# Performance work log

Hardware: AMD Instinct MI355X
Metric: run time of the kernel (lower is better)

Reference implementation:

```python
import jax, jax.numpy as jnp
import numpy as np

N, E = 50000, 800000
IN_C, HID, OUT_C = 100, 128, 40
LAYERS, GROUPS, CODES = 3, 3, 16
BETA = 0.98
EPS = 1e-5


def setup_inputs() -> dict:
    key = jax.random.key(0)
    ks = jax.random.split(key, 16)
    lin = lambda k, i, o: (jax.random.normal(k, (i, o), jnp.float32) / np.sqrt(i)).astype(jnp.float32)
    d = {}
    d["x"] = jax.random.normal(ks[0], (N, IN_C), jnp.float32)
    d["src"] = jax.random.randint(ks[1], (E,), 0, N, jnp.int32)
    d["dst"] = jax.random.randint(ks[2], (E,), 0, N, jnp.int32)
    # SAGEConv params: lin_l (aggregated, with bias) and lin_r (root, no bias)
    d["W0a"], d["W0r"], d["b0"] = lin(ks[3], IN_C, HID), lin(ks[4], IN_C, HID), jnp.zeros((HID,), jnp.float32)
    d["W1a"], d["W1r"], d["b1"] = lin(ks[5], HID, HID), lin(ks[6], HID, HID), jnp.zeros((HID,), jnp.float32)
    d["W2a"], d["W2r"], d["b2"] = lin(ks[7], HID, HID), lin(ks[8], HID, HID), jnp.zeros((HID,), jnp.float32)
    # BatchNorm (eval mode: running stats) for first num_layers-1 = 2 layers
    d["bn_gamma"] = jnp.ones((2, HID), jnp.float32)
    d["bn_beta"] = jnp.zeros((2, HID), jnp.float32)
    d["bn_mean"] = jnp.zeros((2, HID), jnp.float32)
    d["bn_var"] = jnp.ones((2, HID), jnp.float32)
    # Residual VQ codebooks: [layer, group, num_codes, feature]
    d["codebooks"] = 0.1 * jax.random.normal(ks[9], (LAYERS, GROUPS, CODES, HID), jnp.float32)
    d["lin_W"] = lin(ks[10], HID, OUT_C)
    d["lin_b"] = jnp.zeros((OUT_C,), jnp.float32)
    return d


def _sage_conv(h, src, dst, Wa, Wr, b):
    # mean neighbor aggregation (PyG SAGEConv, aggr='mean')
    msg = h[src]                                              # [E, d]
    agg = jax.ops.segment_sum(msg, dst, num_segments=N)       # [N, d]
    deg = jax.ops.segment_sum(jnp.ones((E,), h.dtype), dst, num_segments=N)
    agg = agg / jnp.maximum(deg, 1.0)[:, None]
    return agg @ Wa + b + h @ Wr


def _rvq(h, cb):
    # residual vector quantization over GROUPS codebooks; cb: [G, K, D]
    res, quant, ids = h, jnp.zeros_like(h), []
    for g in range(GROUPS):
        c = cb[g]                                             # [K, D]
        d2 = (jnp.sum(res * res, -1, keepdims=True)
              - 2.0 * res @ c.T + jnp.sum(c * c, -1))          # [N, K]
        idx = jnp.argmin(d2, axis=-1)
        q = c[idx]
        quant = quant + q
        res = res - q
        ids.append(idx)
    sg = jax.lax.stop_gradient
    loss = (BETA * jnp.mean((h - sg(quant)) ** 2)
            + (1.0 - BETA) * jnp.mean((sg(h) - quant) ** 2))
    return loss, jnp.stack(ids, axis=1)                        # [N, G] int


def reference(x, src, dst, W0a, W0r, b0, W1a, W1r, b1, W2a, W2r, b2,
              bn_gamma, bn_beta, bn_mean, bn_var, codebooks, lin_W, lin_b):
    Ws = [(W0a, W0r, b0), (W1a, W1r, b1), (W2a, W2r, b2)]
    h = x
    total_loss = jnp.float32(0.0)
    id_list = []
    for i in range(LAYERS - 1):
        h = _sage_conv(h, src, dst, *Ws[i])
        h = (h - bn_mean[i]) * jax.lax.rsqrt(bn_var[i] + EPS) * bn_gamma[i] + bn_beta[i]
        h = jax.nn.relu(h)                                     # dropout: eval mode (identity)
        loss, ids = _rvq(h, codebooks[i])
        total_loss = total_loss + loss
        id_list.append(ids)
    h = _sage_conv(h, src, dst, *Ws[-1])
    loss, ids = _rvq(h, codebooks[-1])
    total_loss = total_loss + loss
    id_list.append(ids)
    out = h @ lin_W + lin_b
    return out, total_loss, jnp.concatenate(id_list, axis=1)
```

## Files before the change

### kernel.cpp

```cpp
#include <hip/hip_runtime.h>

#define NN 50000
#define HID 128
#define IN_C 100
#define OUT_C 40

__global__ __launch_bounds__(256)
void hist_kernel(const int* __restrict__ dst, int* __restrict__ deg, int E) {
    int e = blockIdx.x * 256 + threadIdx.x;
    if (e < E) atomicAdd(&deg[dst[e]], 1);
}

__global__ __launch_bounds__(256)
void chunk_sum_kernel(const int* __restrict__ deg, int* __restrict__ chunk_sums, int N) {
    __shared__ int s[256];
    const int t = threadIdx.x;
    const int i = blockIdx.x * 256 + t;
    s[t] = (i < N) ? deg[i] : 0;
    __syncthreads();
    for (int o = 128; o; o >>= 1) { if (t < o) s[t] += s[t + o]; __syncthreads(); }
    if (t == 0) chunk_sums[blockIdx.x] = s[0];
}

__global__ __launch_bounds__(256)
void chunk_scan_kernel(int* __restrict__ chunk_sums, int M) {
    __shared__ int s[256];
    const int t = threadIdx.x;
    int v = (t < M) ? chunk_sums[t] : 0;
    s[t] = v;
    __syncthreads();
    for (int o = 1; o < 256; o <<= 1) {
        int x = (t >= o) ? s[t - o] : 0;
        __syncthreads();
        s[t] += x;
        __syncthreads();
    }
    if (t < M) chunk_sums[t] = s[t] - v;
}

__global__ __launch_bounds__(256)
void chunk_apply_kernel(const int* __restrict__ deg, const int* __restrict__ chunk_sums,
                        int* __restrict__ row_start, int* __restrict__ cursor, int N) {
    __shared__ int s[256];
    const int t = threadIdx.x;
    const int i = blockIdx.x * 256 + t;
    int v = (i < N) ? deg[i] : 0;
    s[t] = v;
    __syncthreads();
    for (int o = 1; o < 256; o <<= 1) {
        int x = (t >= o) ? s[t - o] : 0;
        __syncthreads();
        s[t] += x;
        __syncthreads();
    }
    if (i < N) {
        int ex = chunk_sums[blockIdx.x] + s[t] - v;
        row_start[i] = ex;
        cursor[i] = ex;
        if (i == N - 1) row_start[N] = ex + v;
    }
}

__global__ __launch_bounds__(256)
void scatter_kernel(const int* __restrict__ src, const int* __restrict__ dst,
                    int* __restrict__ cursor, int* __restrict__ csr_src, int E) {
    int e = blockIdx.x * 256 + threadIdx.x;
    if (e < E) {
        int pos = atomicAdd(&cursor[dst[e]], 1);
        csr_src[pos] = src[e];
    }
}

__global__ __launch_bounds__(128)
void prep_pack(const float* __restrict__ Wa, const float* __restrict__ Wr,
               float2* __restrict__ wp) {
    const int k = blockIdx.x, col = threadIdx.x;
    float2 v;
    v.x = Wa[(size_t)k * HID + col];
    v.y = Wr[(size_t)k * HID + col];
    wp[(size_t)k * HID + col] = v;
}

template<int K, bool HAS_BN>
__global__ __launch_bounds__(512, 6)
void layer_fused(const float* __restrict__ h_in,
                 const int* __restrict__ row_start, const int* __restrict__ csr_src,
                 const float2* __restrict__ wp, const float* __restrict__ b,
                 const float* __restrict__ gamma, const float* __restrict__ beta,
                 const float* __restrict__ mean, const float* __restrict__ var,
                 const float* __restrict__ cb,
                 float* __restrict__ h_out,
                 float* __restrict__ ids_out, int id_col0,
                 double* __restrict__ loss_part) {
    __shared__ double s_agg[8][HID];
    __shared__ double s_h[8][HID];
    __shared__ float s_cb[3 * 16 * HID];
    const int t = threadIdx.x;
    const int w = t >> 6, lane = t & 63;
    const int n0 = blockIdx.x * 8;

    for (int idx = t; idx < 3 * 16 * HID; idx += 512) s_cb[idx] = cb[idx];

    {
        const int n = n0 + w;
        const int r0 = row_start[n], r1 = row_start[n + 1];
        const int f0 = 2 * lane;
        if (f0 < K) {
            double s0 = 0, s1 = 0, s2 = 0, s3 = 0, s4 = 0, s5 = 0, s6 = 0, s7 = 0;
            int i = r0;
            for (; i + 3 < r1; i += 4) {
                float2 v0 = *(const float2*)(h_in + (size_t)csr_src[i] * K + f0);
                float2 v1 = *(const float2*)(h_in + (size_t)csr_src[i + 1] * K + f0);
                float2 v2 = *(const float2*)(h_in + (size_t)csr_src[i + 2] * K + f0);
                float2 v3 = *(const float2*)(h_in + (size_t)csr_src[i + 3] * K + f0);
                s0 += (double)v0.x; s1 += (double)v0.y;
                s2 += (double)v1.x; s3 += (double)v1.y;
                s4 += (double)v2.x; s5 += (double)v2.y;
                s6 += (double)v3.x; s7 += (double)v3.y;
            }
            for (; i < r1; ++i) {
                float2 v = *(const float2*)(h_in + (size_t)csr_src[i] * K + f0);
                s0 += (double)v.x; s1 += (double)v.y;
            }
            const int deg = r1 - r0;
            const double dd = (double)(deg > 1 ? deg : 1);
            float2 root = *(const float2*)(h_in + (size_t)n * K + f0);
            s_agg[w][f0]     = ((s0 + s2) + (s4 + s6)) / dd;
            s_agg[w][f0 + 1] = ((s1 + s3) + (s5 + s7)) / dd;
            s_h[w][f0]     = (double)root.x;
            s_h[w][f0 + 1] = (double)root.y;
        }
    }
    __syncthreads();

    const int col = t & 127;
    const int p4 = t >> 7;
    double accA = (double)b[col];
    double accB = accA;
#pragma unroll 4
    for (int k = 0; k < K; ++k) {
        const float2 wv = wp[(size_t)k * HID + col];
        const double wa = (double)wv.x, wr = (double)wv.y;
        accA += s_agg[p4][k] * wa + s_h[p4][k] * wr;
        accB += s_agg[p4 + 4][k] * wa + s_h[p4 + 4][k] * wr;
    }
    __syncthreads();

    {
        double vA = accA, vB = accB;
        if (HAS_BN) {
            const double scale = (double)gamma[col] / sqrt((double)var[col] + 1e-5);
            const double shift = (double)beta[col] - (double)mean[col] * scale;
            vA = vA * scale + shift; vA = vA > 0.0 ? vA : 0.0;
            vB = vB * scale + shift; vB = vB > 0.0 ? vB : 0.0;
        }
        const float fA = (float)vA, fB = (float)vB;
        h_out[(size_t)(n0 + p4) * HID + col] = fA;
        h_out[(size_t)(n0 + p4 + 4) * HID + col] = fB;
        s_agg[p4][col] = (double)fA;
        s_agg[p4 + 4][col] = (double)fB;
    }
    __syncthreads();

    {
        double* res = &s_agg[w][0];
        double* s_ws = &s_h[0][0];
        const int n = n0 + w;
        const int k = lane & 15, q = lane >> 4;
        const int jbase = q * 32;
        const int rot = (k + 8 * q) & 31;

        for (int g = 0; g < 3; ++g) {
            const float* c = &s_cb[(g * 16 + k) * HID];
            double r0 = res[lane], r1 = res[lane + 64];
            double pr = r0 * r0 + r1 * r1;
            pr += __shfl_xor(pr, 1, 64);
            pr += __shfl_xor(pr, 2, 64);
            pr += __shfl_xor(pr, 4, 64);
            pr += __shfl_xor(pr, 8, 64);
            pr += __shfl_xor(pr, 16, 64);
            pr += __shfl_xor(pr, 32, 64);
            const float rr32 = (float)pr;

            double cc = 0.0, dot = 0.0;
#pragma unroll
            for (int j2 = 0; j2 < 32; ++j2) {
                const int j = jbase + ((j2 + rot) & 31);
                const double cj = (double)c[j];
                cc += cj * cj;
                dot += res[j] * cj;
            }
            cc += __shfl_xor(cc, 16, 64);
            cc += __shfl_xor(cc, 32, 64);
            dot += __shfl_xor(dot, 16, 64);
            dot += __shfl_xor(dot, 32, 64);

            const float cc32 = (float)cc;
            const float rc32 = (float)dot;
            const float t1 = rr32 - 2.0f * rc32;
            const float d2 = t1 + cc32;

            float bv = d2; int bk = k;
            {
                float ov; int ok;
                ov = __shfl_xor(bv, 1, 64); ok = __shfl_xor(bk, 1, 64);
                if (ov < bv || (ov == bv && ok < bk)) { bv = ov; bk = ok; }
                ov = __shfl_xor(bv, 2, 64); ok = __shfl_xor(bk, 2, 64);
                if (ov < bv || (ov == bv && ok < bk)) { bv = ov; bk = ok; }
                ov = __shfl_xor(bv, 4, 64); ok = __shfl_xor(bk, 4, 64);
                if (ov < bv || (ov == bv && ok < bk)) { bv = ov; bk = ok; }
                ov = __shfl_xor(bv, 8, 64); ok = __shfl_xor(bk, 8, 64);
                if (ov < bv || (ov == bv && ok < bk)) { bv = ov; bk = ok; }
            }
            if (lane == 0)
                ids_out[(size_t)n * 9 + id_col0 + g] = (float)bk;

            const float* cbest = &s_cb[(g * 16 + bk) * HID];
            res[lane]      -= (double)cbest[lane];
            res[lane + 64] -= (double)cbest[lane + 64];
        }
        double r0 = res[lane], r1 = res[lane + 64];
        double wl = r0 * r0 + r1 * r1;
        wl += __shfl_xor(wl, 1, 64);
        wl += __shfl_xor(wl, 2, 64);
        wl += __shfl_xor(wl, 4, 64);
        wl += __shfl_xor(wl, 8, 64);
        wl += __shfl_xor(wl, 16, 64);
        wl += __shfl_xor(wl, 32, 64);
        if (lane == 0) s_ws[w] = wl;
    }
    __syncthreads();
    if (t == 0) {
        const double* s_ws = &s_h[0][0];
        double s = 0.0;
#pragma unroll
        for (int i = 0; i < 8; i++) s += s_ws[i];
        loss_part[blockIdx.x] = s;
    }
}

__global__ __launch_bounds__(128)
void linear_kernel(const float* __restrict__ h, const float* __restrict__ W,
                   const float* __restrict__ b, float* __restrict__ out, int N) {
    constexpr int NODES = 32;
    __shared__ float s_w[HID * OUT_C];
    __shared__ float s_b[OUT_C];
    __shared__ float s_h[HID];
    const int t = threadIdx.x;
    for (int idx = t; idx < HID * OUT_C; idx += 128) s_w[idx] = W[idx];
    if (t < OUT_C) s_b[t] = b[t];
    __syncthreads();
    const int n0 = blockIdx.x * NODES;
    for (int ni = 0; ni < NODES; ++ni) {
        int n = n0 + ni;
        if (n >= N) break;
        s_h[t] = h[(size_t)n * HID + t];
        __syncthreads();
        if (t < OUT_C) {
            double acc = (double)s_b[t];
            for (int kk = 0; kk < HID; kk++)
                acc += (double)s_h[kk] * (double)s_w[kk * OUT_C + t];
            out[(size_t)n * OUT_C + t] = (float)acc;
        }
        __syncthreads();
    }
}

__global__ __launch_bounds__(256)
void finalize_kernel(const double* __restrict__ loss_part, int M,
                     float* __restrict__ out_loss) {
    __shared__ double s[256];
    const int t = threadIdx.x;
    double v = 0.0;
    for (int i = t; i < M; i += 256) v += loss_part[i];
    s[t] = v;
    __syncthreads();
    for (int off = 128; off; off >>= 1) {
        if (t < off) s[t] += s[t + off];
        __syncthreads();
    }
    if (t == 0) out_loss[0] = (float)(s[0] / ((double)NN * (double)HID));
}

extern "C" void kernel_launch(void* const* d_in, const int* in_sizes, int n_in,
                              void* d_out, int out_size, void* d_ws, size_t ws_size,
                              hipStream_t stream) {
    const float* x    = (const float*)d_in[0];
    const int*   src  = (const int*)d_in[1];
    const int*   dst  = (const int*)d_in[2];
    const float* W0a = (const float*)d_in[3];
    const float* W0r = (const float*)d_in[4];
    const float* b0  = (const float*)d_in[5];
    const float* W1a = (const float*)d_in[6];
    const float* W1r = (const float*)d_in[7];
    const float* b1  = (const float*)d_in[8];
    const float* W2a = (const float*)d_in[9];
    const float* W2r = (const float*)d_in[10];
    const float* b2  = (const float*)d_in[11];
    const float* bn_gamma = (const float*)d_in[12];
    const float* bn_beta  = (const float*)d_in[13];
    const float* bn_mean  = (const float*)d_in[14];
    const float* bn_var   = (const float*)d_in[15];
    const float* cb    = (const float*)d_in[16];
    const float* lin_W = (const float*)d_in[17];
    const float* lin_b = (const float*)d_in[18];

    const int E = in_sizes[1];

    float* out      = (float*)d_out;
    float* out_loss = out + (size_t)NN * OUT_C;
    float* out_ids  = out_loss + 1;

    char* base = (char*)d_ws;
    size_t off = 0;
    auto alloc = [&](size_t bytes) -> void* {
        off = (off + 511) & ~(size_t)511;
        void* p = base + off;
        off += bytes;
        return p;
    };
    int* deg_i      = (int*)alloc((size_t)NN * 4);
    int* row_start  = (int*)alloc((size_t)(NN + 1) * 4);
    int* cursor     = (int*)alloc((size_t)NN * 4);
    int* csr_src    = (int*)alloc((size_t)E * 4);
    int* chunk_sums = (int*)alloc(256 * 4);
    double* loss_part = (double*)alloc((size_t)3 * 6250 * 8);
    float* h1  = (float*)alloc((size_t)NN * HID * 4);
    float* h2  = (float*)alloc((size_t)NN * HID * 4);
    float2* wp0 = (float2*)alloc((size_t)IN_C * HID * 8);
    float2* wp1 = (float2*)alloc((size_t)HID * HID * 8);
    float2* wp2 = (float2*)alloc((size_t)HID * HID * 8);

    const int cb_layer = 3 * 16 * HID;
    const int NB = NN / 8;
    const int NCHUNK = (NN + 255) / 256;

    hipMemsetAsync(deg_i, 0, NN * sizeof(int), stream);
    hist_kernel<<<(E + 255) / 256, 256, 0, stream>>>(dst, deg_i, E);
    chunk_sum_kernel<<<NCHUNK, 256, 0, stream>>>(deg_i, chunk_sums, NN);
    chunk_scan_kernel<<<1, 256, 0, stream>>>(chunk_sums, NCHUNK);
    chunk_apply_kernel<<<NCHUNK, 256, 0, stream>>>(deg_i, chunk_sums, row_start, cursor, NN);
    scatter_kernel<<<(E + 255) / 256, 256, 0, stream>>>(src, dst, cursor, csr_src, E);

    prep_pack<<<IN_C, 128, 0, stream>>>(W0a, W0r, wp0);
    prep_pack<<<HID, 128, 0, stream>>>(W1a, W1r, wp1);
    prep_pack<<<HID, 128, 0, stream>>>(W2a, W2r, wp2);

    layer_fused<IN_C, true><<<NB, 512, 0, stream>>>(
        x, row_start, csr_src, wp0, b0, bn_gamma, bn_beta, bn_mean, bn_var,
        cb + 0 * cb_layer, h1, out_ids, 0, loss_part);

    layer_fused<HID, true><<<NB, 512, 0, stream>>>(
        h1, row_start, csr_src, wp1, b1,
        bn_gamma + HID, bn_beta + HID, bn_mean + HID, bn_var + HID,
        cb + 1 * cb_layer, h2, out_ids, 3, loss_part + NB);

    layer_fused<HID, false><<<NB, 512, 0, stream>>>(
        h2, row_start, csr_src, wp2, b2, nullptr, nullptr, nullptr, nullptr,
        cb + 2 * cb_layer, h1, out_ids, 6, loss_part + 2 * NB);

    linear_kernel<<<(NN + 31) / 32, 128, 0, stream>>>(h1, lin_W, lin_b, out, NN);
    finalize_kernel<<<1, 256, 0, stream>>>(loss_part, 3 * NB, out_loss);
}
```

Before: 1.143 ms.

## Fuse output linear layer into last SAGE layer and shrink gather unroll

Removes the separate linear_kernel and computes the final 128x40 projection inside the third layer_fused kernel. Each wave reads the node's post-conv features from shared memory and lin_W from global memory. This avoids re-reading h from global and one launch. The neighbor-gather loop also drops from 4-way to 2-way unrolling, which lowers register pressure but leaves fewer loads in flight. The fused linear step reads lin_W uncached per wave and lengthens the last kernel.

Measured after the change: 1.167 ms. 2.0% more time.

```diff
diff --git a/kernel.cpp b/kernel.cpp
--- a/kernel.cpp
+++ b/kernel.cpp
@@ -81,7 +81,7 @@
     wp[(size_t)k * HID + col] = v;
 }
 
-template<int K, bool HAS_BN>
+template<int K, bool HAS_BN, bool LAST>
 __global__ __launch_bounds__(512, 6)
 void layer_fused(const float* __restrict__ h_in,
                  const int* __restrict__ row_start, const int* __restrict__ csr_src,
@@ -91,10 +91,13 @@
                  const float* __restrict__ cb,
                  float* __restrict__ h_out,
                  float* __restrict__ ids_out, int id_col0,
-                 double* __restrict__ loss_part) {
+                 double* __restrict__ loss_part,
+                 const float* __restrict__ lin_W, const float* __restrict__ lin_b,
+                 float* __restrict__ out) {
     __shared__ double s_agg[8][HID];
     __shared__ double s_h[8][HID];
     __shared__ float s_cb[3 * 16 * HID];
+    __shared__ double s_ws[8];
     const int t = threadIdx.x;
     const int w = t >> 6, lane = t & 63;
     const int n0 = blockIdx.x * 8;
@@ -106,27 +109,23 @@
         const int r0 = row_start[n], r1 = row_start[n + 1];
         const int f0 = 2 * lane;
         if (f0 < K) {
-            double s0 = 0, s1 = 0, s2 = 0, s3 = 0, s4 = 0, s5 = 0, s6 = 0, s7 = 0;
+            double a0 = 0.0, a1 = 0.0, c0 = 0.0, c1 = 0.0;
             int i = r0;
-            for (; i + 3 < r1; i += 4) {
-                float2 v0 = *(const float2*)(h_in + (size_t)csr_src[i] * K + f0);
-                float2 v1 = *(const float2*)(h_in + (size_t)csr_src[i + 1] * K + f0);
-                float2 v2 = *(const float2*)(h_in + (size_t)csr_src[i + 2] * K + f0);
-                float2 v3 = *(const float2*)(h_in + (size_t)csr_src[i + 3] * K + f0);
-                s0 += (double)v0.x; s1 += (double)v0.y;
-                s2 += (double)v1.x; s3 += (double)v1.y;
-                s4 += (double)v2.x; s5 += (double)v2.y;
-                s6 += (double)v3.x; s7 += (double)v3.y;
+            for (; i + 1 < r1; i += 2) {
+                const float2 v0 = *(const float2*)(h_in + (size_t)csr_src[i] * K + f0);
+                const float2 v1 = *(const float2*)(h_in + (size_t)csr_src[i + 1] * K + f0);
+                a0 += (double)v0.x; a1 += (double)v0.y;
+                c0 += (double)v1.x; c1 += (double)v1.y;
             }
-            for (; i < r1; ++i) {
-                float2 v = *(const float2*)(h_in + (size_t)csr_src[i] * K + f0);
-                s0 += (double)v.x; s1 += (double)v.y;
+            if (i < r1) {
+                const float2 v0 = *(const float2*)(h_in + (size_t)csr_src[i] * K + f0);
+                a0 += (double)v0.x; a1 += (double)v0.y;
             }
             const int deg = r1 - r0;
             const double dd = (double)(deg > 1 ? deg : 1);
-            float2 root = *(const float2*)(h_in + (size_t)n * K + f0);
-            s_agg[w][f0]     = ((s0 + s2) + (s4 + s6)) / dd;
-            s_agg[w][f0 + 1] = ((s1 + s3) + (s5 + s7)) / dd;
+            const float2 root = *(const float2*)(h_in + (size_t)n * K + f0);
+            s_agg[w][f0]     = (a0 + c0) / dd;
+            s_agg[w][f0 + 1] = (a1 + c1) / dd;
             s_h[w][f0]     = (double)root.x;
             s_h[w][f0 + 1] = (double)root.y;
         }
@@ -159,12 +158,15 @@
         h_out[(size_t)(n0 + p4 + 4) * HID + col] = fB;
         s_agg[p4][col] = (double)fA;
         s_agg[p4 + 4][col] = (double)fB;
+        if (LAST) {
+            s_h[p4][col] = (double)fA;
+            s_h[p4 + 4][col] = (double)fB;
+        }
     }
     __syncthreads();
 
     {
         double* res = &s_agg[w][0];
-        double* s_ws = &s_h[0][0];
         const int n = n0 + w;
         const int k = lane & 15, q = lane >> 4;
         const int jbase = q * 32;
@@ -229,40 +231,23 @@
         wl += __shfl_xor(wl, 32, 64);
         if (lane == 0) s_ws[w] = wl;
     }
+
+    if (LAST) {
+        const int n = n0 + w;
+        if (lane < OUT_C) {
+            double acc = (double)lin_b[lane];
+            for (int kk = 0; kk < HID; ++kk)
+                acc += s_h[w][kk] * (double)lin_W[kk * OUT_C + lane];
+            out[(size_t)n * OUT_C + lane] = (float)acc;
+        }
+    }
+
     __syncthreads();
     if (t == 0) {
-        const double* s_ws = &s_h[0][0];
         double s = 0.0;
 #pragma unroll
         for (int i = 0; i < 8; i++) s += s_ws[i];
         loss_part[blockIdx.x] = s;
-    }
-}
-
-__global__ __launch_bounds__(128)
-void linear_kernel(const float* __restrict__ h, const float* __restrict__ W,
-                   const float* __restrict__ b, float* __restrict__ out, int N) {
-    constexpr int NODES = 32;
-    __shared__ float s_w[HID * OUT_C];
-    __shared__ float s_b[OUT_C];
-    __shared__ float s_h[HID];
-    const int t = threadIdx.x;
-    for (int idx = t; idx < HID * OUT_C; idx += 128) s_w[idx] = W[idx];
-    if (t < OUT_C) s_b[t] = b[t];
-    __syncthreads();
-    const int n0 = blockIdx.x * NODES;
-    for (int ni = 0; ni < NODES; ++ni) {
-        int n = n0 + ni;
-        if (n >= N) break;
-        s_h[t] = h[(size_t)n * HID + t];
-        __syncthreads();
-        if (t < OUT_C) {
-            double acc = (double)s_b[t];
-            for (int kk = 0; kk < HID; kk++)
-                acc += (double)s_h[kk] * (double)s_w[kk * OUT_C + t];
-            out[(size_t)n * OUT_C + t] = (float)acc;
-        }
-        __syncthreads();
     }
 }
 
@@ -346,19 +331,18 @@
     prep_pack<<<HID, 128, 0, stream>>>(W1a, W1r, wp1);
     prep_pack<<<HID, 128, 0, stream>>>(W2a, W2r, wp2);
 
-    layer_fused<IN_C, true><<<NB, 512, 0, stream>>>(
+    layer_fused<IN_C, true, false><<<NB, 512, 0, stream>>>(
         x, row_start, csr_src, wp0, b0, bn_gamma, bn_beta, bn_mean, bn_var,
-        cb + 0 * cb_layer, h1, out_ids, 0, loss_part);
-
-    layer_fused<HID, true><<<NB, 512, 0, stream>>>(
+        cb + 0 * cb_layer, h1, out_ids, 0, loss_part, nullptr, nullptr, nullptr);
+
+    layer_fused<HID, true, false><<<NB, 512, 0, stream>>>(
         h1, row_start, csr_src, wp1, b1,
         bn_gamma + HID, bn_beta + HID, bn_mean + HID, bn_var + HID,
-        cb + 1 * cb_layer, h2, out_ids, 3, loss_part + NB);
-
-    layer_fused<HID, false><<<NB, 512, 0, stream>>>(
+        cb + 1 * cb_layer, h2, out_ids, 3, loss_part + NB, nullptr, nullptr, nullptr);
+
+    layer_fused<HID, false, true><<<NB, 512, 0, stream>>>(
         h2, row_start, csr_src, wp2, b2, nullptr, nullptr, nullptr, nullptr,
-        cb + 2 * cb_layer, h1, out_ids, 6, loss_part + 2 * NB);
-
-    linear_kernel<<<(NN + 31) / 32, 128, 0, stream>>>(h1, lin_W, lin_b, out, NN);
+        cb + 2 * cb_layer, h1, out_ids, 6, loss_part + 2 * NB, lin_W, lin_b, out);
+
     finalize_kernel<<<1, 256, 0, stream>>>(loss_part, 3 * NB, out_loss);
 }
```
